# Performance work log

Measured on AMD Instinct MI355X. Metric: run time of the kernel, lower is better.

Reference implementation:

```python
import jax, jax.numpy as jnp
import numpy as np

N = 50000      # num_nodes
E = 800000     # num_edges (before self-loops)
IN = 512       # in_channels
HID = 64       # hidden_channels
H = 8          # num_heads (layer 1)
OUT = 128      # out_channels
NEG_SLOPE = 0.2


def setup_inputs() -> dict:
    key = jax.random.key(0)
    ks = jax.random.split(key, 10)
    x = jax.random.normal(ks[0], (N, IN), jnp.float32)
    edge_index = jax.random.randint(ks[1], (2, E), 0, N, jnp.int32)

    def glorot(k, shape):
        fan_in, fan_out = shape[0], int(np.prod(shape[1:]))
        s = jnp.sqrt(2.0 / (fan_in + fan_out)).astype(jnp.float32)
        return jax.random.normal(k, shape, jnp.float32) * s

    # layer 1: GATConv(IN -> HID, heads=H, concat=True)
    W1 = glorot(ks[2], (IN, H * HID))
    att_src1 = glorot(ks[3], (H, HID))
    att_dst1 = glorot(ks[4], (H, HID))
    b1 = jnp.zeros((H * HID,), jnp.float32)
    # layer 2: GATConv(H*HID -> OUT, heads=1, concat=False)
    W2 = glorot(ks[5], (H * HID, OUT))
    att_src2 = glorot(ks[6], (1, OUT))
    att_dst2 = glorot(ks[7], (1, OUT))
    b2 = jnp.zeros((OUT,), jnp.float32)
    return {"x": x, "edge_index": edge_index,
            "W1": W1, "b1": b1, "att_src1": att_src1, "att_dst1": att_dst1,
            "W2": W2, "b2": b2, "att_src2": att_src2, "att_dst2": att_dst2}


def gat_layer(x, src, dst, W, b, a_src, a_dst, heads, concat):
    n = x.shape[0]
    h = (x @ W).reshape(n, heads, -1)                     # [N, H, C]
    e_src = (h * a_src).sum(-1)                           # [N, H]
    e_dst = (h * a_dst).sum(-1)                           # [N, H]
    e = jax.nn.leaky_relu(e_src[src] + e_dst[dst], NEG_SLOPE)   # [E, H]
    # segment softmax over incoming edges of each destination node
    m = jax.ops.segment_max(e, dst, num_segments=n)       # [N, H]
    m = jnp.where(jnp.isneginf(m), 0.0, m)                # empty segments
    p = jnp.exp(e - m[dst])                               # [E, H]
    s = jax.ops.segment_sum(p, dst, num_segments=n)       # [N, H]
    alpha = p / (s[dst] + 1e-16)                          # [E, H]
    out = jax.ops.segment_sum(alpha[..., None] * h[src], dst, num_segments=n)  # [N, H, C]
    if concat:
        return out.reshape(n, -1) + b
    return out.mean(axis=1) + b


def reference(x, edge_index, W1, b1, att_src1, att_dst1, W2, b2, att_src2, att_dst2):
    # PyG GATConv adds self-loops by default
    loops = jnp.arange(N, dtype=edge_index.dtype)
    src = jnp.concatenate([edge_index[0], loops])
    dst = jnp.concatenate([edge_index[1], loops])
    h = gat_layer(x, src, dst, W1, b1, att_src1, att_dst1, H, True)   # [N, H*HID]
    h = jax.nn.relu(h)
    out = gat_layer(h, src, dst, W2, b2, att_src2, att_dst2, 1, False)  # [N, OUT]
    return out
```

## Files before the change

kernel.cpp:

```cpp
#include <hip/hip_runtime.h>
#include <hip/hip_fp16.h>

#define NNODES 50000
#define NEDGES 800000
#define ETOT   (NNODES + NEDGES)
#define NH     8
#define HID    64
#define D1     512
#define INC    512
#define OUTC   128
#define NEG    0.2f
#define MPAD   50048

typedef __attribute__((ext_vector_type(8))) short short8;
typedef __attribute__((ext_vector_type(4))) float f32x4;
typedef _Float16 half8v __attribute__((ext_vector_type(8)));
typedef _Float16 half2v __attribute__((ext_vector_type(2)));

__device__ __forceinline__ ushort f2h_bits(float x) {
    _Float16 h = (_Float16)x; return __builtin_bit_cast(ushort, h);
}
__device__ __forceinline__ float h2f(ushort b) {
    return (float)__builtin_bit_cast(_Float16, b);
}
__device__ __forceinline__ uint splat_h2(float p) {
    uint b = (uint)f2h_bits(p); return b | (b << 16);
}
__device__ __forceinline__ half2v as_h2(uint u) { return __builtin_bit_cast(half2v, u); }
__device__ __forceinline__ float leaky(float v) { return v >= 0.f ? v : NEG * v; }

__global__ void count_deg(const int* __restrict__ ei, int* __restrict__ deg) {
    int i = blockIdx.x * 256 + threadIdx.x;
    if (i >= ETOT) return;
    int dst = (i < NEDGES) ? ei[NEDGES + i] : (i - NEDGES);
    atomicAdd(&deg[dst], 1);
}

__global__ void scan_deg(const int* __restrict__ deg, int* __restrict__ rs) {
    __shared__ int part[1024];
    const int n = NNODES;
    const int CH = (n + 1023) / 1024;
    int t = threadIdx.x;
    int lo = t * CH, hi = min(lo + CH, n);
    int s = 0;
    for (int i = lo; i < hi; ++i) s += deg[i];
    part[t] = s;
    __syncthreads();
    for (int off = 1; off < 1024; off <<= 1) {
        int v = (t >= off) ? part[t - off] : 0;
        __syncthreads();
        part[t] += v;
        __syncthreads();
    }
    int run = (t == 0) ? 0 : part[t - 1];
    for (int i = lo; i < hi; ++i) { rs[i] = run; run += deg[i]; }
    if (hi == n) rs[n] = run;
}

__global__ void scatter_edges(const int* __restrict__ ei, int* __restrict__ cursor,
                              int* __restrict__ csr_src) {
    int i = blockIdx.x * 256 + threadIdx.x;
    if (i >= ETOT) return;
    int src, dst;
    if (i < NEDGES) { src = ei[i]; dst = ei[NEDGES + i]; }
    else            { src = dst = i - NEDGES; }
    int pos = atomicAdd(&cursor[dst], 1);
    csr_src[pos] = src;
}

__global__ void cast_f16(const float* __restrict__ x, ushort* __restrict__ xh, int n4) {
    int i = blockIdx.x * 256 + threadIdx.x;
    if (i >= n4) return;
    float4 v = *(const float4*)&x[(size_t)i * 4];
    ushort4 o = { f2h_bits(v.x), f2h_bits(v.y), f2h_bits(v.z), f2h_bits(v.w) };
    *(ushort4*)&xh[(size_t)i * 4] = o;
}

__global__ void cast_wT(const float* __restrict__ W, ushort* __restrict__ WT, int K, int N) {
    int idx = blockIdx.x * 256 + threadIdx.x;
    if (idx >= K * N) return;
    int n = idx / K, k = idx - n * K;
    WT[idx] = f2h_bits(W[(size_t)k * N + n]);
}

template<int KDIM>
__global__ __launch_bounds__(256) void gemm_f16(const ushort* __restrict__ A,
                                                const ushort* __restrict__ Bt,
                                                ushort* __restrict__ C,
                                                int M, int N) {
    __shared__ __align__(16) ushort Asl[128 * 64];
    __shared__ __align__(16) ushort Bsl[128 * 64];
    const int tid  = threadIdx.x;
    const int lane = tid & 63;
    const int wid  = tid >> 6;
    const int wr   = wid >> 1, wc = wid & 1;
    const int fr   = lane & 15, fq = lane >> 4;
    const int m0   = blockIdx.x * 128;
    const int n0   = blockIdx.y * 128;

    f32x4 acc[4][4] = {};

    for (int k0 = 0; k0 < KDIM; k0 += 64) {
        __syncthreads();
        #pragma unroll
        for (int i = 0; i < 4; ++i) {
            int chunk = wid * 4 + i;
            int r = chunk * 8 + (lane >> 3);
            const ushort* ga = A  + (size_t)(m0 + r) * KDIM + k0 + (lane & 7) * 8;
            const ushort* gb = Bt + (size_t)(n0 + r) * KDIM + k0 + (lane & 7) * 8;
            __builtin_amdgcn_global_load_lds(
                (const __attribute__((address_space(1))) void*)ga,
                (__attribute__((address_space(3))) void*)(Asl + chunk * 512), 16, 0, 0);
            __builtin_amdgcn_global_load_lds(
                (const __attribute__((address_space(1))) void*)gb,
                (__attribute__((address_space(3))) void*)(Bsl + chunk * 512), 16, 0, 0);
        }
        __syncthreads();
        #pragma unroll
        for (int ks = 0; ks < 2; ++ks) {
            short8 a[4], b[4];
            #pragma unroll
            for (int m = 0; m < 4; ++m)
                a[m] = *(const short8*)&Asl[(wr * 64 + m * 16 + fr) * 64 + ks * 32 + fq * 8];
            #pragma unroll
            for (int n = 0; n < 4; ++n)
                b[n] = *(const short8*)&Bsl[(wc * 64 + n * 16 + fr) * 64 + ks * 32 + fq * 8];
            #pragma unroll
            for (int m = 0; m < 4; ++m)
                #pragma unroll
                for (int n = 0; n < 4; ++n)
                    acc[m][n] = __builtin_amdgcn_mfma_f32_16x16x32_f16(
                        __builtin_bit_cast(half8v, a[m]),
                        __builtin_bit_cast(half8v, b[n]), acc[m][n], 0, 0, 0);
        }
    }
    #pragma unroll
    for (int m = 0; m < 4; ++m) {
        #pragma unroll
        for (int r = 0; r < 4; ++r) {
            int row = m0 + wr * 64 + m * 16 + fq * 4 + r;
            if (row >= M) continue;
            #pragma unroll
            for (int n = 0; n < 4; ++n)
                C[(size_t)row * N + n0 + wc * 64 + n * 16 + fr] = f2h_bits(acc[m][n][r]);
        }
    }
}

__global__ void dots1(const ushort* __restrict__ h1, const float* __restrict__ a_src,
                      const float* __restrict__ a_dst,
                      float* __restrict__ es, float* __restrict__ ed) {
    int gw   = (blockIdx.x * blockDim.x + threadIdx.x) >> 6;
    int lane = threadIdx.x & 63;
    if (gw >= NNODES) return;
    short8 v = *(const short8*)&h1[(size_t)gw * D1 + lane * 8];
    half8v hv = __builtin_bit_cast(half8v, v);
    int h = lane >> 3, c0 = (lane & 7) * 8;
    float s = 0.f, d = 0.f;
    #pragma unroll
    for (int j = 0; j < 8; ++j) {
        float x = (float)hv[j];
        s += x * a_src[h * HID + c0 + j];
        d += x * a_dst[h * HID + c0 + j];
    }
    #pragma unroll
    for (int off = 1; off < 8; off <<= 1) {
        s += __shfl_xor(s, off);
        d += __shfl_xor(d, off);
    }
    if ((lane & 7) == 0) { es[gw * NH + h] = s; ed[gw * NH + h] = d; }
}

__global__ void dots2(const ushort* __restrict__ h2, const float* __restrict__ a_src,
                      const float* __restrict__ a_dst,
                      float* __restrict__ es, float* __restrict__ ed) {
    int gw   = (blockIdx.x * blockDim.x + threadIdx.x) >> 6;
    int lane = threadIdx.x & 63;
    if (gw >= NNODES) return;
    uint u = *(const uint*)&h2[(size_t)gw * OUTC + lane * 2];
    float x0 = h2f((ushort)(u & 0xffffu)), x1 = h2f((ushort)(u >> 16));
    float s = x0 * a_src[lane * 2] + x1 * a_src[lane * 2 + 1];
    float d = x0 * a_dst[lane * 2] + x1 * a_dst[lane * 2 + 1];
    #pragma unroll
    for (int off = 1; off < 64; off <<= 1) {
        s += __shfl_xor(s, off);
        d += __shfl_xor(d, off);
    }
    if (lane == 0) { es[gw] = s; ed[gw] = d; }
}

#define CAP1 128
__global__ __launch_bounds__(256) void attn1(const ushort* __restrict__ h1,
                                             const float* __restrict__ esrc,
                                             const float* __restrict__ edst,
                                             const int* __restrict__ rs,
                                             const int* __restrict__ csr_src,
                                             const float* __restrict__ b1,
                                             ushort* __restrict__ out1) {
    int t = threadIdx.x;
    int lane = t & 63, wid = t >> 6;
    int nidx = wid >> 1, wv = wid & 1;
    int n = blockIdx.x * 2 + nidx;
    int beg = rs[n], deg = rs[n + 1] - beg;
    int dcap = min(deg, CAP1);
    __shared__ float alpha_sh[2][CAP1][NH];
    __shared__ int   ssrc_sh[2][CAP1];
    __shared__ float msh[2][NH], rinv_sh[2][NH];

    {
        int e0 = t & 127;
        for (int e = e0; e < dcap; e += 128) ssrc_sh[nidx][e] = csr_src[beg + e];
    }
    __syncthreads();

    {
        int h0 = wv * 4;
        float4 ed4 = *(const float4*)&edst[n * NH + h0];
        float m0 = -1e30f, m1 = -1e30f, m2 = -1e30f, m3 = -1e30f;
        for (int e = lane; e < deg; e += 64) {
            int s = (e < CAP1) ? ssrc_sh[nidx][e] : csr_src[beg + e];
            float4 es4 = *(const float4*)&esrc[s * NH + h0];
            float v0 = leaky(es4.x + ed4.x), v1 = leaky(es4.y + ed4.y);
            float v2 = leaky(es4.z + ed4.z), v3 = leaky(es4.w + ed4.w);
            if (e < CAP1) {
                float4 vv = { v0, v1, v2, v3 };
                *(float4*)&alpha_sh[nidx][e][h0] = vv;
            }
            m0 = fmaxf(m0, v0); m1 = fmaxf(m1, v1);
            m2 = fmaxf(m2, v2); m3 = fmaxf(m3, v3);
        }
        #pragma unroll
        for (int off = 32; off; off >>= 1) {
            m0 = fmaxf(m0, __shfl_xor(m0, off));
            m1 = fmaxf(m1, __shfl_xor(m1, off));
            m2 = fmaxf(m2, __shfl_xor(m2, off));
            m3 = fmaxf(m3, __shfl_xor(m3, off));
        }
        float s0 = 0.f, s1 = 0.f, s2 = 0.f, s3 = 0.f;
        for (int e = lane; e < deg; e += 64) {
            float v0, v1, v2, v3;
            if (e < CAP1) {
                float4 vv = *(const float4*)&alpha_sh[nidx][e][h0];
                v0 = vv.x; v1 = vv.y; v2 = vv.z; v3 = vv.w;
            } else {
                int s = csr_src[beg + e];
                float4 es4 = *(const float4*)&esrc[s * NH + h0];
                v0 = leaky(es4.x + ed4.x); v1 = leaky(es4.y + ed4.y);
                v2 = leaky(es4.z + ed4.z); v3 = leaky(es4.w + ed4.w);
            }
            float p0 = __expf(v0 - m0), p1 = __expf(v1 - m1);
            float p2 = __expf(v2 - m2), p3 = __expf(v3 - m3);
            if (e < CAP1) {
                uint4 pk = { splat_h2(p0), splat_h2(p1), splat_h2(p2), splat_h2(p3) };
                *(uint4*)&alpha_sh[nidx][e][h0] = pk;
            }
            s0 += p0; s1 += p1; s2 += p2; s3 += p3;
        }
        #pragma unroll
        for (int off = 32; off; off >>= 1) {
            s0 += __shfl_xor(s0, off); s1 += __shfl_xor(s1, off);
            s2 += __shfl_xor(s2, off); s3 += __shfl_xor(s3, off);
        }
        if (lane == 0) {
            msh[nidx][h0] = m0; msh[nidx][h0 + 1] = m1;
            msh[nidx][h0 + 2] = m2; msh[nidx][h0 + 3] = m3;
            rinv_sh[nidx][h0]     = 1.f / (s0 + 1e-16f);
            rinv_sh[nidx][h0 + 1] = 1.f / (s1 + 1e-16f);
            rinv_sh[nidx][h0 + 2] = 1.f / (s2 + 1e-16f);
            rinv_sh[nidx][h0 + 3] = 1.f / (s3 + 1e-16f);
        }
    }
    __syncthreads();

    int tt = t & 127;
    int c0 = tt * 4;
    int h = tt >> 4;
    float m = msh[nidx][h], ri = rinv_sh[nidx][h];
    float edn = edst[n * NH + h];
    half2v a01 = {}, a01b = {}, a23 = {}, a23b = {};
    const int* ss = ssrc_sh[nidx];
    int e = 0;
    for (; e + 4 <= dcap; e += 4) {
        int s0i = ss[e], s1i = ss[e + 1], s2i = ss[e + 2], s3i = ss[e + 3];
        uint2 u0 = *(const uint2*)&h1[(size_t)s0i * D1 + c0];
        uint2 u1 = *(const uint2*)&h1[(size_t)s1i * D1 + c0];
        uint2 u2 = *(const uint2*)&h1[(size_t)s2i * D1 + c0];
        uint2 u3 = *(const uint2*)&h1[(size_t)s3i * D1 + c0];
        half2v p0 = as_h2(*(const uint*)&alpha_sh[nidx][e][h]);
        half2v p1 = as_h2(*(const uint*)&alpha_sh[nidx][e + 1][h]);
        half2v p2 = as_h2(*(const uint*)&alpha_sh[nidx][e + 2][h]);
        half2v p3 = as_h2(*(const uint*)&alpha_sh[nidx][e + 3][h]);
        a01  = as_h2(u0.x) * p0 + a01;  a23  = as_h2(u0.y) * p0 + a23;
        a01b = as_h2(u1.x) * p1 + a01b; a23b = as_h2(u1.y) * p1 + a23b;
        a01  = as_h2(u2.x) * p2 + a01;  a23  = as_h2(u2.y) * p2 + a23;
        a01b = as_h2(u3.x) * p3 + a01b; a23b = as_h2(u3.y) * p3 + a23b;
    }
    for (; e < dcap; ++e) {
        int s = ss[e];
        uint2 u = *(const uint2*)&h1[(size_t)s * D1 + c0];
        half2v p = as_h2(*(const uint*)&alpha_sh[nidx][e][h]);
        a01 = as_h2(u.x) * p + a01;
        a23 = as_h2(u.y) * p + a23;
    }
    for (; e < deg; ++e) {
        int s = csr_src[beg + e];
        float p = __expf(leaky(esrc[s * NH + h] + edn) - m);
        half2v ph = as_h2(splat_h2(p));
        uint2 u = *(const uint2*)&h1[(size_t)s * D1 + c0];
        a01 = as_h2(u.x) * ph + a01;
        a23 = as_h2(u.y) * ph + a23;
    }
    float ac0 = (float)a01[0] + (float)a01b[0];
    float ac1 = (float)a01[1] + (float)a01b[1];
    float ac2 = (float)a23[0] + (float)a23b[0];
    float ac3 = (float)a23[1] + (float)a23b[1];
    float4 bb = *(const float4*)&b1[c0];
    float o0 = fmaxf(ac0 * ri + bb.x, 0.f);
    float o1 = fmaxf(ac1 * ri + bb.y, 0.f);
    float o2 = fmaxf(ac2 * ri + bb.z, 0.f);
    float o3 = fmaxf(ac3 * ri + bb.w, 0.f);
    uint2 pkout;
    pkout.x = (uint)f2h_bits(o0) | ((uint)f2h_bits(o1) << 16);
    pkout.y = (uint)f2h_bits(o2) | ((uint)f2h_bits(o3) << 16);
    *(uint2*)&out1[(size_t)n * D1 + c0] = pkout;
}

#define CAP2 128
__global__ __launch_bounds__(256) void attn2(const ushort* __restrict__ h2,
                                             const float* __restrict__ esrc,
                                             const float* __restrict__ edst,
                                             const int* __restrict__ rs,
                                             const int* __restrict__ csr_src,
                                             const float* __restrict__ b2,
                                             float* __restrict__ out) {
    int t = threadIdx.x;
    int g = t >> 5, lane32 = t & 31;
    int n = blockIdx.x * 8 + g;
    if (n >= NNODES) return;
    int beg = rs[n], deg = rs[n + 1] - beg;
    int dcap = min(deg, CAP2);
    __shared__ float al_sh[8][CAP2];
    __shared__ int   ss_sh[8][CAP2];
    float* al = al_sh[g];
    int*   ss = ss_sh[g];

    for (int e = lane32; e < dcap; e += 32) ss[e] = csr_src[beg + e];

    float edn = edst[n];
    float m = -1e30f;
    for (int e = lane32; e < deg; e += 32) {
        int s = (e < CAP2) ? ss[e] : csr_src[beg + e];
        float v = leaky(esrc[s] + edn);
        if (e < CAP2) al[e] = v;
        m = fmaxf(m, v);
    }
    #pragma unroll
    for (int off = 16; off; off >>= 1) m = fmaxf(m, __shfl_xor(m, off));
    float ssum = 0.f;
    for (int e = lane32; e < deg; e += 32) {
        float v = (e < CAP2) ? al[e] : leaky(esrc[csr_src[beg + e]] + edn);
        float p = __expf(v - m);
        if (e < CAP2) *(uint*)&al[e] = splat_h2(p);
        ssum += p;
    }
    #pragma unroll
    for (int off = 16; off; off >>= 1) ssum += __shfl_xor(ssum, off);
    float ri = 1.f / (ssum + 1e-16f);

    int c0 = lane32 * 4;
    half2v a01 = {}, a01b = {}, a23 = {}, a23b = {};
    int e = 0;
    for (; e + 4 <= dcap; e += 4) {
        int s0i = ss[e], s1i = ss[e + 1], s2i = ss[e + 2], s3i = ss[e + 3];
        uint2 u0 = *(const uint2*)&h2[(size_t)s0i * OUTC + c0];
        uint2 u1 = *(const uint2*)&h2[(size_t)s1i * OUTC + c0];
        uint2 u2 = *(const uint2*)&h2[(size_t)s2i * OUTC + c0];
        uint2 u3 = *(const uint2*)&h2[(size_t)s3i * OUTC + c0];
        half2v p0 = as_h2(*(const uint*)&al[e]);
        half2v p1 = as_h2(*(const uint*)&al[e + 1]);
        half2v p2 = as_h2(*(const uint*)&al[e + 2]);
        half2v p3 = as_h2(*(const uint*)&al[e + 3]);
        a01  = as_h2(u0.x) * p0 + a01;  a23  = as_h2(u0.y) * p0 + a23;
        a01b = as_h2(u1.x) * p1 + a01b; a23b = as_h2(u1.y) * p1 + a23b;
        a01  = as_h2(u2.x) * p2 + a01;  a23  = as_h2(u2.y) * p2 + a23;
        a01b = as_h2(u3.x) * p3 + a01b; a23b = as_h2(u3.y) * p3 + a23b;
    }
    for (; e < dcap; ++e) {
        int s = ss[e];
        uint2 u = *(const uint2*)&h2[(size_t)s * OUTC + c0];
        half2v p = as_h2(*(const uint*)&al[e]);
        a01 = as_h2(u.x) * p + a01;
        a23 = as_h2(u.y) * p + a23;
    }
    for (; e < deg; ++e) {
        int s = csr_src[beg + e];
        float p = __expf(leaky(esrc[s] + edn) - m);
        half2v ph = as_h2(splat_h2(p));
        uint2 u = *(const uint2*)&h2[(size_t)s * OUTC + c0];
        a01 = as_h2(u.x) * ph + a01;
        a23 = as_h2(u.y) * ph + a23;
    }
    float4 bb = *(const float4*)&b2[c0];
    float4 o;
    o.x = ((float)a01[0] + (float)a01b[0]) * ri + bb.x;
    o.y = ((float)a01[1] + (float)a01b[1]) * ri + bb.y;
    o.z = ((float)a23[0] + (float)a23b[0]) * ri + bb.z;
    o.w = ((float)a23[1] + (float)a23b[1]) * ri + bb.w;
    *(float4*)&out[(size_t)n * OUTC + c0] = o;
}

extern "C" void kernel_launch(void* const* d_in, const int* in_sizes, int n_in,
                              void* d_out, int out_size, void* d_ws, size_t ws_size,
                              hipStream_t stream) {
    const float* x   = (const float*)d_in[0];
    const int*   ei  = (const int*)  d_in[1];
    const float* W1  = (const float*)d_in[2];
    const float* b1  = (const float*)d_in[3];
    const float* as1 = (const float*)d_in[4];
    const float* ad1 = (const float*)d_in[5];
    const float* W2  = (const float*)d_in[6];
    const float* b2  = (const float*)d_in[7];
    const float* as2 = (const float*)d_in[8];
    const float* ad2 = (const float*)d_in[9];
    float* out = (float*)d_out;

    char* ws = (char*)d_ws;
    size_t off = 0;
    auto alloc = [&](size_t bytes) -> void* {
        void* p = ws + off;
        off = (off + bytes + 255) & ~(size_t)255;
        return p;
    };
    ushort* xh    = (ushort*)alloc((size_t)MPAD * INC * 2);
    ushort* w1t   = (ushort*)alloc((size_t)D1 * INC * 2);
    ushort* w2t   = (ushort*)alloc((size_t)OUTC * D1 * 2);
    ushort* h1h   = (ushort*)alloc((size_t)MPAD * D1 * 2);
    ushort* out1h = (ushort*)alloc((size_t)MPAD * D1 * 2);
    ushort* h2h   = (ushort*)alloc((size_t)MPAD * OUTC * 2);
    float*  es1   = (float*)alloc((size_t)NNODES * NH * 4);
    float*  ed1   = (float*)alloc((size_t)NNODES * NH * 4);
    float*  es2   = (float*)alloc((size_t)NNODES * 4);
    float*  ed2   = (float*)alloc((size_t)NNODES * 4);
    int*    deg   = (int*)alloc((size_t)NNODES * 4);
    int*    rs    = (int*)alloc((size_t)(NNODES + 1) * 4);
    int*    cur   = (int*)alloc((size_t)NNODES * 4);
    int*    csr   = (int*)alloc((size_t)ETOT * 4);

    hipMemsetAsync(deg, 0, (size_t)NNODES * 4, stream);
    count_deg<<<(ETOT + 255) / 256, 256, 0, stream>>>(ei, deg);
    scan_deg<<<1, 1024, 0, stream>>>(deg, rs);
    hipMemcpyAsync(cur, rs, (size_t)NNODES * 4, hipMemcpyDeviceToDevice, stream);
    scatter_edges<<<(ETOT + 255) / 256, 256, 0, stream>>>(ei, cur, csr);

    cast_f16<<<(NNODES * INC / 4 + 255) / 256, 256, 0, stream>>>(x, xh, NNODES * INC / 4);
    cast_wT<<<(INC * D1 + 255) / 256, 256, 0, stream>>>(W1, w1t, INC, D1);
    cast_wT<<<(D1 * OUTC + 255) / 256, 256, 0, stream>>>(W2, w2t, D1, OUTC);

    gemm_f16<INC><<<dim3(MPAD / 128, D1 / 128), 256, 0, stream>>>(xh, w1t, h1h, NNODES, D1);
    dots1<<<(NNODES * 64 + 255) / 256, 256, 0, stream>>>(h1h, as1, ad1, es1, ed1);
    attn1<<<NNODES / 2, 256, 0, stream>>>(h1h, es1, ed1, rs, csr, b1, out1h);

    gemm_f16<D1><<<dim3(MPAD / 128, OUTC / 128), 256, 0, stream>>>(out1h, w2t, h2h, NNODES, OUTC);
    dots2<<<(NNODES * 64 + 255) / 256, 256, 0, stream>>>(h2h, as2, ad2, es2, ed2);
    attn2<<<NNODES / 8, 256, 0, stream>>>(h2h, es2, ed2, rs, csr, b2, out);
}
```

Before: 591.2 us.

## Swizzle GEMM LDS layout and map one wavefront per node in attn1

The GEMM's global-to-LDS loads and MFMA fragment reads now use an XOR swizzle on the 16-byte column slot, to cut LDS bank conflicts on the fragment reads. attn1 is restructured so that a single 64-lane wavefront handles each destination node across all 8 heads. Each lane gathers 16-byte rows instead of 8-byte ones, and the block-level __syncthreads are removed, with four nodes per block. The per-wave softmax keeps 8 heads of state per lane, which raises register pressure, and the alpha buffer is padded to 9 words per row to avoid bank conflicts.

```diff
diff --git a/kernel.cpp b/kernel.cpp
--- a/kernel.cpp
+++ b/kernel.cpp
@@ -100,14 +100,16 @@
 
     f32x4 acc[4][4] = {};
 
+    const int gcol = (((lane & 7) ^ ((lane >> 3) & 7))) * 8;
+
     for (int k0 = 0; k0 < KDIM; k0 += 64) {
         __syncthreads();
         #pragma unroll
         for (int i = 0; i < 4; ++i) {
             int chunk = wid * 4 + i;
             int r = chunk * 8 + (lane >> 3);
-            const ushort* ga = A  + (size_t)(m0 + r) * KDIM + k0 + (lane & 7) * 8;
-            const ushort* gb = Bt + (size_t)(n0 + r) * KDIM + k0 + (lane & 7) * 8;
+            const ushort* ga = A  + (size_t)(m0 + r) * KDIM + k0 + gcol;
+            const ushort* gb = Bt + (size_t)(n0 + r) * KDIM + k0 + gcol;
             __builtin_amdgcn_global_load_lds(
                 (const __attribute__((address_space(1))) void*)ga,
                 (__attribute__((address_space(3))) void*)(Asl + chunk * 512), 16, 0, 0);
@@ -120,11 +122,17 @@
         for (int ks = 0; ks < 2; ++ks) {
             short8 a[4], b[4];
             #pragma unroll
-            for (int m = 0; m < 4; ++m)
-                a[m] = *(const short8*)&Asl[(wr * 64 + m * 16 + fr) * 64 + ks * 32 + fq * 8];
+            for (int m = 0; m < 4; ++m) {
+                int row = wr * 64 + m * 16 + fr;
+                int slot = (ks * 4 + fq) ^ (fr & 7);
+                a[m] = *(const short8*)&Asl[row * 64 + slot * 8];
+            }
             #pragma unroll
-            for (int n = 0; n < 4; ++n)
-                b[n] = *(const short8*)&Bsl[(wc * 64 + n * 16 + fr) * 64 + ks * 32 + fq * 8];
+            for (int n = 0; n < 4; ++n) {
+                int row = wc * 64 + n * 16 + fr;
+                int slot = (ks * 4 + fq) ^ (fr & 7);
+                b[n] = *(const short8*)&Bsl[row * 64 + slot * 8];
+            }
             #pragma unroll
             for (int m = 0; m < 4; ++m)
                 #pragma unroll
@@ -197,132 +205,124 @@
                                              const int* __restrict__ csr_src,
                                              const float* __restrict__ b1,
                                              ushort* __restrict__ out1) {
-    int t = threadIdx.x;
-    int lane = t & 63, wid = t >> 6;
-    int nidx = wid >> 1, wv = wid & 1;
-    int n = blockIdx.x * 2 + nidx;
+    int t = threadIdx.x, lane = t & 63, w = t >> 6;
+    int n = blockIdx.x * 4 + w;
     int beg = rs[n], deg = rs[n + 1] - beg;
     int dcap = min(deg, CAP1);
-    __shared__ float alpha_sh[2][CAP1][NH];
-    __shared__ int   ssrc_sh[2][CAP1];
-    __shared__ float msh[2][NH], rinv_sh[2][NH];
-
-    {
-        int e0 = t & 127;
-        for (int e = e0; e < dcap; e += 128) ssrc_sh[nidx][e] = csr_src[beg + e];
-    }
-    __syncthreads();
-
-    {
-        int h0 = wv * 4;
-        float4 ed4 = *(const float4*)&edst[n * NH + h0];
-        float m0 = -1e30f, m1 = -1e30f, m2 = -1e30f, m3 = -1e30f;
-        for (int e = lane; e < deg; e += 64) {
-            int s = (e < CAP1) ? ssrc_sh[nidx][e] : csr_src[beg + e];
-            float4 es4 = *(const float4*)&esrc[s * NH + h0];
-            float v0 = leaky(es4.x + ed4.x), v1 = leaky(es4.y + ed4.y);
-            float v2 = leaky(es4.z + ed4.z), v3 = leaky(es4.w + ed4.w);
-            if (e < CAP1) {
-                float4 vv = { v0, v1, v2, v3 };
-                *(float4*)&alpha_sh[nidx][e][h0] = vv;
-            }
-            m0 = fmaxf(m0, v0); m1 = fmaxf(m1, v1);
-            m2 = fmaxf(m2, v2); m3 = fmaxf(m3, v3);
-        }
-        #pragma unroll
-        for (int off = 32; off; off >>= 1) {
-            m0 = fmaxf(m0, __shfl_xor(m0, off));
-            m1 = fmaxf(m1, __shfl_xor(m1, off));
-            m2 = fmaxf(m2, __shfl_xor(m2, off));
-            m3 = fmaxf(m3, __shfl_xor(m3, off));
-        }
-        float s0 = 0.f, s1 = 0.f, s2 = 0.f, s3 = 0.f;
-        for (int e = lane; e < deg; e += 64) {
-            float v0, v1, v2, v3;
-            if (e < CAP1) {
-                float4 vv = *(const float4*)&alpha_sh[nidx][e][h0];
-                v0 = vv.x; v1 = vv.y; v2 = vv.z; v3 = vv.w;
-            } else {
-                int s = csr_src[beg + e];
-                float4 es4 = *(const float4*)&esrc[s * NH + h0];
-                v0 = leaky(es4.x + ed4.x); v1 = leaky(es4.y + ed4.y);
-                v2 = leaky(es4.z + ed4.z); v3 = leaky(es4.w + ed4.w);
-            }
-            float p0 = __expf(v0 - m0), p1 = __expf(v1 - m1);
-            float p2 = __expf(v2 - m2), p3 = __expf(v3 - m3);
-            if (e < CAP1) {
-                uint4 pk = { splat_h2(p0), splat_h2(p1), splat_h2(p2), splat_h2(p3) };
-                *(uint4*)&alpha_sh[nidx][e][h0] = pk;
-            }
-            s0 += p0; s1 += p1; s2 += p2; s3 += p3;
-        }
-        #pragma unroll
-        for (int off = 32; off; off >>= 1) {
-            s0 += __shfl_xor(s0, off); s1 += __shfl_xor(s1, off);
-            s2 += __shfl_xor(s2, off); s3 += __shfl_xor(s3, off);
-        }
-        if (lane == 0) {
-            msh[nidx][h0] = m0; msh[nidx][h0 + 1] = m1;
-            msh[nidx][h0 + 2] = m2; msh[nidx][h0 + 3] = m3;
-            rinv_sh[nidx][h0]     = 1.f / (s0 + 1e-16f);
-            rinv_sh[nidx][h0 + 1] = 1.f / (s1 + 1e-16f);
-            rinv_sh[nidx][h0 + 2] = 1.f / (s2 + 1e-16f);
-            rinv_sh[nidx][h0 + 3] = 1.f / (s3 + 1e-16f);
-        }
-    }
-    __syncthreads();
-
-    int tt = t & 127;
-    int c0 = tt * 4;
-    int h = tt >> 4;
-    float m = msh[nidx][h], ri = rinv_sh[nidx][h];
-    float edn = edst[n * NH + h];
-    half2v a01 = {}, a01b = {}, a23 = {}, a23b = {};
-    const int* ss = ssrc_sh[nidx];
+    __shared__ uint  alpha_sh[4][CAP1][9];
+    __shared__ int   ssrc_sh[4][CAP1];
+    uint (*alpha)[9] = alpha_sh[w];
+    int* ss = ssrc_sh[w];
+
+    for (int e = lane; e < dcap; e += 64) ss[e] = csr_src[beg + e];
+
+    float4 edA = *(const float4*)&edst[n * NH];
+    float4 edB = *(const float4*)&edst[n * NH + 4];
+    float mx[8], sm[8];
+    #pragma unroll
+    for (int h = 0; h < 8; ++h) { mx[h] = -1e30f; sm[h] = 0.f; }
+
+    for (int e = lane; e < deg; e += 64) {
+        int s = (e < CAP1) ? ss[e] : csr_src[beg + e];
+        float4 eA = *(const float4*)&esrc[(size_t)s * NH];
+        float4 eB = *(const float4*)&esrc[(size_t)s * NH + 4];
+        float v[8] = { leaky(eA.x + edA.x), leaky(eA.y + edA.y),
+                       leaky(eA.z + edA.z), leaky(eA.w + edA.w),
+                       leaky(eB.x + edB.x), leaky(eB.y + edB.y),
+                       leaky(eB.z + edB.z), leaky(eB.w + edB.w) };
+        #pragma unroll
+        for (int h = 0; h < 8; ++h) {
+            if (e < CAP1) alpha[e][h] = __float_as_uint(v[h]);
+            mx[h] = fmaxf(mx[h], v[h]);
+        }
+    }
+    #pragma unroll
+    for (int off = 1; off < 64; off <<= 1)
+        #pragma unroll
+        for (int h = 0; h < 8; ++h)
+            mx[h] = fmaxf(mx[h], __shfl_xor(mx[h], off));
+
+    for (int e = lane; e < deg; e += 64) {
+        float v[8];
+        if (e < CAP1) {
+            #pragma unroll
+            for (int h = 0; h < 8; ++h) v[h] = __uint_as_float(alpha[e][h]);
+        } else {
+            int s = csr_src[beg + e];
+            float4 eA = *(const float4*)&esrc[(size_t)s * NH];
+            float4 eB = *(const float4*)&esrc[(size_t)s * NH + 4];
+            v[0] = leaky(eA.x + edA.x); v[1] = leaky(eA.y + edA.y);
+            v[2] = leaky(eA.z + edA.z); v[3] = leaky(eA.w + edA.w);
+            v[4] = leaky(eB.x + edB.x); v[5] = leaky(eB.y + edB.y);
+            v[6] = leaky(eB.z + edB.z); v[7] = leaky(eB.w + edB.w);
+        }
+        #pragma unroll
+        for (int h = 0; h < 8; ++h) {
+            float p = __expf(v[h] - mx[h]);
+            if (e < CAP1) alpha[e][h] = splat_h2(p);
+            sm[h] += p;
+        }
+    }
+    #pragma unroll
+    for (int off = 1; off < 64; off <<= 1)
+        #pragma unroll
+        for (int h = 0; h < 8; ++h)
+            sm[h] += __shfl_xor(sm[h], off);
+
+    int h = lane >> 3;
+    float mm = mx[0], ssv = sm[0], edn = edA.x;
+    float edv[8] = { edA.x, edA.y, edA.z, edA.w, edB.x, edB.y, edB.z, edB.w };
+    #pragma unroll
+    for (int hh = 1; hh < 8; ++hh)
+        if (h == hh) { mm = mx[hh]; ssv = sm[hh]; edn = edv[hh]; }
+    float ri = 1.f / (ssv + 1e-16f);
+
+    int c0 = lane * 8;
+    half2v aA0 = {}, aA1 = {}, aA2 = {}, aA3 = {};
+    half2v aB0 = {}, aB1 = {}, aB2 = {}, aB3 = {};
     int e = 0;
-    for (; e + 4 <= dcap; e += 4) {
-        int s0i = ss[e], s1i = ss[e + 1], s2i = ss[e + 2], s3i = ss[e + 3];
-        uint2 u0 = *(const uint2*)&h1[(size_t)s0i * D1 + c0];
-        uint2 u1 = *(const uint2*)&h1[(size_t)s1i * D1 + c0];
-        uint2 u2 = *(const uint2*)&h1[(size_t)s2i * D1 + c0];
-        uint2 u3 = *(const uint2*)&h1[(size_t)s3i * D1 + c0];
-        half2v p0 = as_h2(*(const uint*)&alpha_sh[nidx][e][h]);
-        half2v p1 = as_h2(*(const uint*)&alpha_sh[nidx][e + 1][h]);
-        half2v p2 = as_h2(*(const uint*)&alpha_sh[nidx][e + 2][h]);
-        half2v p3 = as_h2(*(const uint*)&alpha_sh[nidx][e + 3][h]);
-        a01  = as_h2(u0.x) * p0 + a01;  a23  = as_h2(u0.y) * p0 + a23;
-        a01b = as_h2(u1.x) * p1 + a01b; a23b = as_h2(u1.y) * p1 + a23b;
-        a01  = as_h2(u2.x) * p2 + a01;  a23  = as_h2(u2.y) * p2 + a23;
-        a01b = as_h2(u3.x) * p3 + a01b; a23b = as_h2(u3.y) * p3 + a23b;
+    for (; e + 2 <= dcap; e += 2) {
+        int s0i = ss[e], s1i = ss[e + 1];
+        uint4 u0 = *(const uint4*)&h1[(size_t)s0i * D1 + c0];
+        uint4 u1 = *(const uint4*)&h1[(size_t)s1i * D1 + c0];
+        half2v p0 = as_h2(alpha[e][h]);
+        half2v p1 = as_h2(alpha[e + 1][h]);
+        aA0 = as_h2(u0.x) * p0 + aA0; aA1 = as_h2(u0.y) * p0 + aA1;
+        aA2 = as_h2(u0.z) * p0 + aA2; aA3 = as_h2(u0.w) * p0 + aA3;
+        aB0 = as_h2(u1.x) * p1 + aB0; aB1 = as_h2(u1.y) * p1 + aB1;
+        aB2 = as_h2(u1.z) * p1 + aB2; aB3 = as_h2(u1.w) * p1 + aB3;
     }
     for (; e < dcap; ++e) {
         int s = ss[e];
-        uint2 u = *(const uint2*)&h1[(size_t)s * D1 + c0];
-        half2v p = as_h2(*(const uint*)&alpha_sh[nidx][e][h]);
-        a01 = as_h2(u.x) * p + a01;
-        a23 = as_h2(u.y) * p + a23;
+        uint4 u = *(const uint4*)&h1[(size_t)s * D1 + c0];
+        half2v p = as_h2(alpha[e][h]);
+        aA0 = as_h2(u.x) * p + aA0; aA1 = as_h2(u.y) * p + aA1;
+        aA2 = as_h2(u.z) * p + aA2; aA3 = as_h2(u.w) * p + aA3;
     }
     for (; e < deg; ++e) {
         int s = csr_src[beg + e];
-        float p = __expf(leaky(esrc[s * NH + h] + edn) - m);
+        float p = __expf(leaky(esrc[(size_t)s * NH + h] + edn) - mm);
         half2v ph = as_h2(splat_h2(p));
-        uint2 u = *(const uint2*)&h1[(size_t)s * D1 + c0];
-        a01 = as_h2(u.x) * ph + a01;
-        a23 = as_h2(u.y) * ph + a23;
-    }
-    float ac0 = (float)a01[0] + (float)a01b[0];
-    float ac1 = (float)a01[1] + (float)a01b[1];
-    float ac2 = (float)a23[0] + (float)a23b[0];
-    float ac3 = (float)a23[1] + (float)a23b[1];
-    float4 bb = *(const float4*)&b1[c0];
-    float o0 = fmaxf(ac0 * ri + bb.x, 0.f);
-    float o1 = fmaxf(ac1 * ri + bb.y, 0.f);
-    float o2 = fmaxf(ac2 * ri + bb.z, 0.f);
-    float o3 = fmaxf(ac3 * ri + bb.w, 0.f);
-    uint2 pkout;
-    pkout.x = (uint)f2h_bits(o0) | ((uint)f2h_bits(o1) << 16);
-    pkout.y = (uint)f2h_bits(o2) | ((uint)f2h_bits(o3) << 16);
-    *(uint2*)&out1[(size_t)n * D1 + c0] = pkout;
+        uint4 u = *(const uint4*)&h1[(size_t)s * D1 + c0];
+        aA0 = as_h2(u.x) * ph + aA0; aA1 = as_h2(u.y) * ph + aA1;
+        aA2 = as_h2(u.z) * ph + aA2; aA3 = as_h2(u.w) * ph + aA3;
+    }
+    float4 bb0 = *(const float4*)&b1[c0];
+    float4 bb1 = *(const float4*)&b1[c0 + 4];
+    float o0 = fmaxf(((float)aA0[0] + (float)aB0[0]) * ri + bb0.x, 0.f);
+    float o1 = fmaxf(((float)aA0[1] + (float)aB0[1]) * ri + bb0.y, 0.f);
+    float o2 = fmaxf(((float)aA1[0] + (float)aB1[0]) * ri + bb0.z, 0.f);
+    float o3 = fmaxf(((float)aA1[1] + (float)aB1[1]) * ri + bb0.w, 0.f);
+    float o4 = fmaxf(((float)aA2[0] + (float)aB2[0]) * ri + bb1.x, 0.f);
+    float o5 = fmaxf(((float)aA2[1] + (float)aB2[1]) * ri + bb1.y, 0.f);
+    float o6 = fmaxf(((float)aA3[0] + (float)aB3[0]) * ri + bb1.z, 0.f);
+    float o7 = fmaxf(((float)aA3[1] + (float)aB3[1]) * ri + bb1.w, 0.f);
+    uint4 pk;
+    pk.x = (uint)f2h_bits(o0) | ((uint)f2h_bits(o1) << 16);
+    pk.y = (uint)f2h_bits(o2) | ((uint)f2h_bits(o3) << 16);
+    pk.z = (uint)f2h_bits(o4) | ((uint)f2h_bits(o5) << 16);
+    pk.w = (uint)f2h_bits(o6) | ((uint)f2h_bits(o7) << 16);
+    *(uint4*)&out1[(size_t)n * D1 + c0] = pk;
 }
 
 #define CAP2 128
@@ -458,7 +458,7 @@
 
     gemm_f16<INC><<<dim3(MPAD / 128, D1 / 128), 256, 0, stream>>>(xh, w1t, h1h, NNODES, D1);
     dots1<<<(NNODES * 64 + 255) / 256, 256, 0, stream>>>(h1h, as1, ad1, es1, ed1);
-    attn1<<<NNODES / 2, 256, 0, stream>>>(h1h, es1, ed1, rs, csr, b1, out1h);
+    attn1<<<NNODES / 4, 256, 0, stream>>>(h1h, es1, ed1, rs, csr, b1, out1h);
 
     gemm_f16<D1><<<dim3(MPAD / 128, OUTC / 128), 256, 0, stream>>>(out1h, w2t, h2h, NNODES, OUTC);
     dots2<<<(NNODES * 64 + 255) / 256, 256, 0, stream>>>(h2h, as2, ad2, es2, ed2);
```

Result: no change. 590.1 us (-0.2%).
